# Kernel tuning notes

Measured on AMD Instinct MI355X. Metric: run time of the kernel, lower is better.

The kernel has to match this reference:

```python
import jax, jax.numpy as jnp
import numpy as np

H = 8          # kernel_size == hidden size
NUM_LAYERS = 4
NEG_SLOPE = 0.2


def _gru_scan(x_pre, W_hh, b_hh, reverse):
    """Run a single-direction GRU over time.
    x_pre: (N, T, 3H) precomputed input projections W_ih @ x + b_ih.
    Returns outputs (N, T, H) aligned with input time order.
    PyTorch gate order: [r, z, n].
    """
    N = x_pre.shape[0]

    def step(h, xp):
        gh = h @ W_hh.T + b_hh                      # (N, 3H)
        xr, xz, xn = jnp.split(xp, 3, axis=-1)
        hr, hz, hn = jnp.split(gh, 3, axis=-1)
        r = jax.nn.sigmoid(xr + hr)
        z = jax.nn.sigmoid(xz + hz)
        n = jnp.tanh(xn + r * hn)
        h_new = (1.0 - z) * n + z * h
        return h_new, h_new

    h0 = jnp.zeros((N, H), x_pre.dtype)
    _, ys = jax.lax.scan(step, h0, jnp.swapaxes(x_pre, 0, 1), reverse=reverse)
    return jnp.swapaxes(ys, 0, 1)                   # (N, T, H)


def setup_inputs() -> dict:
    key = jax.random.key(0)
    ks = jax.random.split(key, 16)
    s = 1.0 / np.sqrt(H)  # PyTorch GRU init scale
    u = lambda k, shape: jax.random.uniform(k, shape, jnp.float32, -s, s)
    return {
        "raw": jax.random.normal(ks[0], (32, 400, 4096), jnp.float32),
        "W_ih_l0": u(ks[1], (2, 3 * H, H)),
        "W_hh_l0": u(ks[2], (2, 3 * H, H)),
        "b_ih_l0": u(ks[3], (2, 3 * H)),
        "b_hh_l0": u(ks[4], (2, 3 * H)),
        "W_ih_rest": u(ks[5], (NUM_LAYERS - 1, 2, 3 * H, 2 * H)),
        "W_hh_rest": u(ks[6], (NUM_LAYERS - 1, 2, 3 * H, H)),
        "b_ih_rest": u(ks[7], (NUM_LAYERS - 1, 2, 3 * H)),
        "b_hh_rest": u(ks[8], (NUM_LAYERS - 1, 2, 3 * H)),
        "lin1_w": u(ks[9], (H, 2 * H)),
        "lin1_b": u(ks[10], (H,)),
        "lin2_w": u(ks[11], (H, H)),
        "lin2_b": u(ks[12], (H,)),
    }


def reference(raw, W_ih_l0, W_hh_l0, b_ih_l0, b_hh_l0,
              W_ih_rest, W_hh_rest, b_ih_rest, b_hh_rest,
              lin1_w, lin1_b, lin2_w, lin2_b):
    b, k, L = raw.shape
    T = L // H
    x = raw.reshape(b * k, T, H)                    # (N, T, H)

    for layer in range(NUM_LAYERS):
        if layer == 0:
            Wih, Whh, bih, bhh = W_ih_l0, W_hh_l0, b_ih_l0, b_hh_l0
        else:
            Wih, Whh = W_ih_rest[layer - 1], W_hh_rest[layer - 1]
            bih, bhh = b_ih_rest[layer - 1], b_hh_rest[layer - 1]
        # precompute input projections for the whole sequence (batched GEMM)
        out_f = _gru_scan(x @ Wih[0].T + bih[0], Whh[0], bhh[0], reverse=False)
        out_b = _gru_scan(x @ Wih[1].T + bih[1], Whh[1], bhh[1], reverse=True)
        x = jnp.concatenate([out_f, out_b], axis=-1)  # (N, T, 2H)

    last = x[:, -1, :].reshape(b, k, 2 * H)
    # Dropout is identity in eval mode.
    h = last @ lin1_w.T + lin1_b
    h = jnp.where(h >= 0, h, NEG_SLOPE * h)         # LeakyReLU(0.2)
    return h @ lin2_w.T + lin2_b                    # (b, k, out_size)
```

## Files before the change

kernel.cpp:

```cpp
#include <hip/hip_runtime.h>
#include <type_traits>

#define DEVINL __device__ __forceinline__

typedef __fp16 f16;
typedef __fp16 f16x2 __attribute__((ext_vector_type(2)));
typedef __fp16 f16x8 __attribute__((ext_vector_type(8)));

constexpr int Hh = 8;
constexpr int G3 = 24;
constexpr int TT = 512;

constexpr float SNEG  = -1.44269504088896340736f;
constexpr float SNEG2 = -2.88539008177792681472f;

DEVINL float dot2(f16x2 a, f16x2 b, float c) {
#if __has_builtin(__builtin_amdgcn_fdot2)
    return __builtin_amdgcn_fdot2(a, b, c, false);
#else
    return fmaf((float)a[1], (float)b[1], fmaf((float)a[0], (float)b[0], c));
#endif
}

template <typename InT, bool TWO_IN>
DEVINL void load_x(f16x2* d, const InT* pf, const InT* pb) {
    if constexpr (std::is_same<InT, float>::value) {
        const float4* p4 = (const float4*)pf;
        float4 v0 = p4[0], v1 = p4[1];
        d[0] = __builtin_amdgcn_cvt_pkrtz(v0.x, v0.y);
        d[1] = __builtin_amdgcn_cvt_pkrtz(v0.z, v0.w);
        d[2] = __builtin_amdgcn_cvt_pkrtz(v1.x, v1.y);
        d[3] = __builtin_amdgcn_cvt_pkrtz(v1.z, v1.w);
    } else {
        f16x8 a = *(const f16x8*)pf;
        d[0] = __builtin_shufflevector(a, a, 0, 1);
        d[1] = __builtin_shufflevector(a, a, 2, 3);
        d[2] = __builtin_shufflevector(a, a, 4, 5);
        d[3] = __builtin_shufflevector(a, a, 6, 7);
        if constexpr (TWO_IN) {
            f16x8 b = *(const f16x8*)pb;
            d[4] = __builtin_shufflevector(b, b, 0, 1);
            d[5] = __builtin_shufflevector(b, b, 2, 3);
            d[6] = __builtin_shufflevector(b, b, 4, 5);
            d[7] = __builtin_shufflevector(b, b, 6, 7);
        }
    }
}

template <typename InT, bool TWO_IN, bool LAST>
__global__ __launch_bounds__(128, 4) void gru_scan(
    const InT* __restrict__ xf,
    const InT* __restrict__ xb,
    const float* __restrict__ Wih,
    const float* __restrict__ Whh,
    const float* __restrict__ bih,
    const float* __restrict__ bhh,
    f16* __restrict__ outF,
    f16* __restrict__ outB,
    float* __restrict__ last,
    int n)
{
    constexpr int IN_DIM = TWO_IN ? 16 : 8;
    constexpr int QW = IN_DIM / 2;

    const int tid   = threadIdx.x;
    const int lane8 = tid & 7;
    const int grp   = tid >> 3;
    const int unit  = blockIdx.x * 16 + grp;
    const int dir   = unit >= n ? 1 : 0;
    const int seq   = unit - dir * n;

    const int g0 = lane8, g1 = 8 + lane8, g2 = 16 + lane8;

    __shared__ __align__(16) f16 hsh[128];
    const int hbase = grp * 8;

    const float* Wd = Wih + (size_t)dir * G3 * IN_DIM;
    f16x2 wi0[QW], wi1[QW], wi2[QW];
#pragma unroll
    for (int q = 0; q < QW; ++q) {
        wi0[q] = __builtin_amdgcn_cvt_pkrtz(Wd[g0 * IN_DIM + 2 * q] * SNEG,
                                            Wd[g0 * IN_DIM + 2 * q + 1] * SNEG);
        wi1[q] = __builtin_amdgcn_cvt_pkrtz(Wd[g1 * IN_DIM + 2 * q] * SNEG,
                                            Wd[g1 * IN_DIM + 2 * q + 1] * SNEG);
        wi2[q] = __builtin_amdgcn_cvt_pkrtz(Wd[g2 * IN_DIM + 2 * q] * SNEG2,
                                            Wd[g2 * IN_DIM + 2 * q + 1] * SNEG2);
    }
    const float* Hd = Whh + (size_t)dir * G3 * Hh;
    f16x2 wh0[Hh / 2], wh1[Hh / 2], wh2[Hh / 2];
#pragma unroll
    for (int q = 0; q < Hh / 2; ++q) {
        wh0[q] = __builtin_amdgcn_cvt_pkrtz(Hd[g0 * Hh + 2 * q] * SNEG,
                                            Hd[g0 * Hh + 2 * q + 1] * SNEG);
        wh1[q] = __builtin_amdgcn_cvt_pkrtz(Hd[g1 * Hh + 2 * q] * SNEG,
                                            Hd[g1 * Hh + 2 * q + 1] * SNEG);
        wh2[q] = __builtin_amdgcn_cvt_pkrtz(Hd[g2 * Hh + 2 * q] * SNEG2,
                                            Hd[g2 * Hh + 2 * q + 1] * SNEG2);
    }
    const float br  = (bih[dir * G3 + g0] + bhh[dir * G3 + g0]) * SNEG;
    const float bz  = (bih[dir * G3 + g1] + bhh[dir * G3 + g1]) * SNEG;
    const float bxn = bih[dir * G3 + g2] * SNEG2;
    const float bhn = bhh[dir * G3 + g2] * SNEG2;

    f16x2 h2[Hh / 2];
#pragma unroll
    for (int q = 0; q < Hh / 2; ++q) h2[q] = f16x2{(f16)0.f, (f16)0.f};
    float hown = 0.f;

    const int t0 = dir ? (TT - 1) : 0;
    const int xstep = dir ? -8 : 8;
    const int ostep = dir ? -8 : 8;
    const InT* xpf = xf + (size_t)(seq * TT + t0) * 8;
    const InT* xpb = TWO_IN ? (xb + (size_t)(seq * TT + t0) * 8)
                            : (const InT*)nullptr;
    f16* op = LAST ? nullptr
                   : (dir ? outB : outF) + (size_t)(seq * TT + t0) * 8 + lane8;

    const int steps = (LAST && dir) ? 1 : TT;

    f16x2 xA[QW], xB[QW];
    load_x<InT, TWO_IN>(xA, xpf, xpb);
    xpf += xstep; if constexpr (TWO_IN) xpb += xstep;
    if (steps > 1) {
        load_x<InT, TWO_IN>(xB, xpf, xpb);
        xpf += xstep; if constexpr (TWO_IN) xpb += xstep;
    }

#define GRU_STEP(XV, PF)                                                      \
    {                                                                         \
        float sr = br, sz = bz, xn = bxn;                                     \
        _Pragma("unroll")                                                     \
        for (int q = 0; q < QW; ++q) {                                        \
            sr = dot2(wi0[q], XV[q], sr);                                     \
            sz = dot2(wi1[q], XV[q], sz);                                     \
            xn = dot2(wi2[q], XV[q], xn);                                     \
        }                                                                     \
        if (PF) {                                                             \
            load_x<InT, TWO_IN>(XV, xpf, xpb);                                \
            xpf += xstep; if constexpr (TWO_IN) xpb += xstep;                 \
        }                                                                     \
        float hn = bhn;                                                       \
        _Pragma("unroll")                                                     \
        for (int q = 0; q < Hh / 2; ++q) {                                    \
            sr = dot2(wh0[q], h2[q], sr);                                     \
            sz = dot2(wh1[q], h2[q], sz);                                     \
            hn = dot2(wh2[q], h2[q], hn);                                     \
        }                                                                     \
        float r  = __builtin_amdgcn_rcpf(1.f + __builtin_amdgcn_exp2f(sr));   \
        float z  = __builtin_amdgcn_rcpf(1.f + __builtin_amdgcn_exp2f(sz));   \
        float vS = fminf(fmaf(r, hn, xn), 60.f);               \
        float e2 = __builtin_amdgcn_exp2f(vS);                                \
        float nn = (1.f - e2) * __builtin_amdgcn_rcpf(1.f + e2);              \
        float hnew = fmaf(z, hown - nn, nn);               \
        hown = hnew;                                                          \
        f16 hf = (f16)hnew;                           \
        if (!LAST) { *op = hf; op += ostep; }                                 \
        hsh[hbase + lane8] = hf;                                              \
        __builtin_amdgcn_wave_barrier();                                      \
        f16x8 hv = *(const f16x8*)&hsh[hbase];                                \
        h2[0] = __builtin_shufflevector(hv, hv, 0, 1);                        \
        h2[1] = __builtin_shufflevector(hv, hv, 2, 3);                        \
        h2[2] = __builtin_shufflevector(hv, hv, 4, 5);                        \
        h2[3] = __builtin_shufflevector(hv, hv, 6, 7);                        \
    }

    int s = 0;
    for (; s + 2 < steps; s += 2) {
        GRU_STEP(xA, true);
        GRU_STEP(xB, true);
    }
    GRU_STEP(xA, false);
    if (steps > 1) GRU_STEP(xB, false);
#undef GRU_STEP

    if (LAST) last[(size_t)seq * 16 + dir * 8 + lane8] = hown;
}

__global__ void head_kernel(const float* __restrict__ last,
                            const float* __restrict__ w1, const float* __restrict__ b1,
                            const float* __restrict__ w2, const float* __restrict__ b2,
                            float* __restrict__ out, int n)
{
    int i = blockIdx.x * blockDim.x + threadIdx.x;
    if (i >= n) return;
    const float* v = last + (size_t)i * 16;
    float h1[8];
#pragma unroll
    for (int j = 0; j < 8; ++j) {
        float a = b1[j];
#pragma unroll
        for (int k = 0; k < 16; ++k) a = fmaf(w1[j * 16 + k], v[k], a);
        h1[j] = a >= 0.f ? a : 0.2f * a;
    }
#pragma unroll
    for (int j = 0; j < 8; ++j) {
        float o = b2[j];
#pragma unroll
        for (int k = 0; k < 8; ++k) o = fmaf(w2[j * 8 + k], h1[k], o);
        out[(size_t)i * 8 + j] = o;
    }
}

extern "C" void kernel_launch(void* const* d_in, const int* in_sizes, int n_in,
                              void* d_out, int out_size, void* d_ws, size_t ws_size,
                              hipStream_t stream)
{
    const float* raw  = (const float*)d_in[0];
    const float* Wih0 = (const float*)d_in[1];
    const float* Whh0 = (const float*)d_in[2];
    const float* bih0 = (const float*)d_in[3];
    const float* bhh0 = (const float*)d_in[4];
    const float* WihR = (const float*)d_in[5];
    const float* WhhR = (const float*)d_in[6];
    const float* bihR = (const float*)d_in[7];
    const float* bhhR = (const float*)d_in[8];
    const float* w1   = (const float*)d_in[9];
    const float* b1   = (const float*)d_in[10];
    const float* w2   = (const float*)d_in[11];
    const float* b2   = (const float*)d_in[12];

    const int n = in_sizes[0] / (TT * Hh);
    const size_t hbE = (size_t)n * TT * 8;
    dim3 blk(128);
    dim3 grid((unsigned)((2 * n) / 16));
    dim3 hblk(256);
    dim3 hgrid((unsigned)((n + 255) / 256));

    f16* AF = (f16*)d_ws;
    f16* AB = AF + hbE;
    f16* BF = AB + hbE;
    f16* BB = BF + hbE;
    float* lastb = (float*)(BB + hbE);

    gru_scan<float, false, false><<<grid, blk, 0, stream>>>(
        raw, (const float*)nullptr, Wih0, Whh0, bih0, bhh0,
        AF, AB, (float*)nullptr, n);
    gru_scan<f16, true, false><<<grid, blk, 0, stream>>>(
        AF, AB, WihR + 0 * 2 * G3 * 16, WhhR + 0 * 2 * G3 * 8,
        bihR + 0 * 2 * G3, bhhR + 0 * 2 * G3, BF, BB, (float*)nullptr, n);
    gru_scan<f16, true, false><<<grid, blk, 0, stream>>>(
        BF, BB, WihR + 1 * 2 * G3 * 16, WhhR + 1 * 2 * G3 * 8,
        bihR + 1 * 2 * G3, bhhR + 1 * 2 * G3, AF, AB, (float*)nullptr, n);
    gru_scan<f16, true, true><<<grid, blk, 0, stream>>>(
        AF, AB, WihR + 2 * 2 * G3 * 16, WhhR + 2 * 2 * G3 * 8,
        bihR + 2 * 2 * G3, bhhR + 2 * 2 * G3,
        (f16*)nullptr, (f16*)nullptr, lastb, n);
    head_kernel<<<hgrid, hblk, 0, stream>>>(
        lastb, w1, b1, w2, b2, (float*)d_out, n);
}
```

Baseline: 1.375 ms.

## Process two sequences per thread group to interleave independent GRU recurrences

Each 8-lane group now advances two independent sequences at once. Blocks drop to 64 threads, and each block still covers 16 units. Interleaving the two dependency chains is meant to hide the latency of the serial dot/exp/rcp/LDS chain through ILP. The cost is fewer waves and higher register pressure per thread, with launch bounds changed to (64,2), which may reduce occupancy. Offsets now use 32-bit ints.

After: 1.422 ms. +3.4%, slower.

```diff
diff --git a/kernel.cpp b/kernel.cpp
--- a/kernel.cpp
+++ b/kernel.cpp
@@ -48,7 +48,7 @@
 }
 
 template <typename InT, bool TWO_IN, bool LAST>
-__global__ __launch_bounds__(128, 4) void gru_scan(
+__global__ __launch_bounds__(64, 2) void gru_scan(
     const InT* __restrict__ xf,
     const InT* __restrict__ xb,
     const float* __restrict__ Wih,
@@ -62,18 +62,20 @@
 {
     constexpr int IN_DIM = TWO_IN ? 16 : 8;
     constexpr int QW = IN_DIM / 2;
+    constexpr int XD = TT * 8;
 
     const int tid   = threadIdx.x;
     const int lane8 = tid & 7;
     const int grp   = tid >> 3;
-    const int unit  = blockIdx.x * 16 + grp;
-    const int dir   = unit >= n ? 1 : 0;
-    const int seq   = unit - dir * n;
+    const int unit0 = blockIdx.x * 16 + grp * 2;
+    const int dir   = unit0 >= n ? 1 : 0;
+    const int seq0  = unit0 - dir * n;
 
     const int g0 = lane8, g1 = 8 + lane8, g2 = 16 + lane8;
 
     __shared__ __align__(16) f16 hsh[128];
-    const int hbase = grp * 8;
+    const int hb0 = grp * 16;
+    const int hb1 = grp * 16 + 8;
 
     const float* Wd = Wih + (size_t)dir * G3 * IN_DIM;
     f16x2 wi0[QW], wi1[QW], wi2[QW];
@@ -102,78 +104,104 @@
     const float bxn = bih[dir * G3 + g2] * SNEG2;
     const float bhn = bhh[dir * G3 + g2] * SNEG2;
 
-    f16x2 h2[Hh / 2];
-#pragma unroll
-    for (int q = 0; q < Hh / 2; ++q) h2[q] = f16x2{(f16)0.f, (f16)0.f};
-    float hown = 0.f;
+    f16x2 h20[Hh / 2], h21[Hh / 2];
+#pragma unroll
+    for (int q = 0; q < Hh / 2; ++q) {
+        h20[q] = f16x2{(f16)0.f, (f16)0.f};
+        h21[q] = f16x2{(f16)0.f, (f16)0.f};
+    }
+    float hown0 = 0.f, hown1 = 0.f;
 
     const int t0 = dir ? (TT - 1) : 0;
     const int xstep = dir ? -8 : 8;
     const int ostep = dir ? -8 : 8;
-    const InT* xpf = xf + (size_t)(seq * TT + t0) * 8;
-    const InT* xpb = TWO_IN ? (xb + (size_t)(seq * TT + t0) * 8)
-                            : (const InT*)nullptr;
-    f16* op = LAST ? nullptr
-                   : (dir ? outB : outF) + (size_t)(seq * TT + t0) * 8 + lane8;
+    int xoff = (seq0 * TT + t0) * 8;
+    int ooff = (seq0 * TT + t0) * 8 + lane8;
+    f16* oP = LAST ? nullptr : (dir ? outB : outF);
 
     const int steps = (LAST && dir) ? 1 : TT;
 
-    f16x2 xA[QW], xB[QW];
-    load_x<InT, TWO_IN>(xA, xpf, xpb);
-    xpf += xstep; if constexpr (TWO_IN) xpb += xstep;
+    f16x2 xA0[QW], xA1[QW], xB0[QW], xB1[QW];
+    load_x<InT, TWO_IN>(xA0, xf + xoff, xb + xoff);
+    load_x<InT, TWO_IN>(xA1, xf + xoff + XD, xb + xoff + XD);
+    xoff += xstep;
     if (steps > 1) {
-        load_x<InT, TWO_IN>(xB, xpf, xpb);
-        xpf += xstep; if constexpr (TWO_IN) xpb += xstep;
-    }
-
-#define GRU_STEP(XV, PF)                                                      \
+        load_x<InT, TWO_IN>(xB0, xf + xoff, xb + xoff);
+        load_x<InT, TWO_IN>(xB1, xf + xoff + XD, xb + xoff + XD);
+        xoff += xstep;
+    }
+
+#define GRU_STEP(X0, X1, PF)                                                  \
     {                                                                         \
-        float sr = br, sz = bz, xn = bxn;                                     \
+        float sr0 = br, sz0 = bz, xn0 = bxn;                                  \
+        float sr1 = br, sz1 = bz, xn1 = bxn;                                  \
         _Pragma("unroll")                                                     \
         for (int q = 0; q < QW; ++q) {                                        \
-            sr = dot2(wi0[q], XV[q], sr);                                     \
-            sz = dot2(wi1[q], XV[q], sz);                                     \
-            xn = dot2(wi2[q], XV[q], xn);                                     \
+            sr0 = dot2(wi0[q], X0[q], sr0);                                   \
+            sz0 = dot2(wi1[q], X0[q], sz0);                                   \
+            xn0 = dot2(wi2[q], X0[q], xn0);                                   \
+            sr1 = dot2(wi0[q], X1[q], sr1);                                   \
+            sz1 = dot2(wi1[q], X1[q], sz1);                                   \
+            xn1 = dot2(wi2[q], X1[q], xn1);                                   \
         }                                                                     \
         if (PF) {                                                             \
-            load_x<InT, TWO_IN>(XV, xpf, xpb);                                \
-            xpf += xstep; if constexpr (TWO_IN) xpb += xstep;                 \
+            load_x<InT, TWO_IN>(X0, xf + xoff, xb + xoff);                    \
+            load_x<InT, TWO_IN>(X1, xf + xoff + XD, xb + xoff + XD);          \
+            xoff += xstep;                                                    \
         }                                                                     \
-        float hn = bhn;                                                       \
+        float hn0 = bhn, hn1 = bhn;                                           \
         _Pragma("unroll")                                                     \
         for (int q = 0; q < Hh / 2; ++q) {                                    \
-            sr = dot2(wh0[q], h2[q], sr);                                     \
-            sz = dot2(wh1[q], h2[q], sz);                                     \
-            hn = dot2(wh2[q], h2[q], hn);                                     \
+            sr0 = dot2(wh0[q], h20[q], sr0);                                  \
+            sz0 = dot2(wh1[q], h20[q], sz0);                                  \
+            hn0 = dot2(wh2[q], h20[q], hn0);                                  \
+            sr1 = dot2(wh0[q], h21[q], sr1);                                  \
+            sz1 = dot2(wh1[q], h21[q], sz1);                                  \
+            hn1 = dot2(wh2[q], h21[q], hn1);                                  \
         }                                                                     \
-        float r  = __builtin_amdgcn_rcpf(1.f + __builtin_amdgcn_exp2f(sr));   \
-        float z  = __builtin_amdgcn_rcpf(1.f + __builtin_amdgcn_exp2f(sz));   \
-        float vS = fminf(fmaf(r, hn, xn), 60.f);               \
-        float e2 = __builtin_amdgcn_exp2f(vS);                                \
-        float nn = (1.f - e2) * __builtin_amdgcn_rcpf(1.f + e2);              \
-        float hnew = fmaf(z, hown - nn, nn);               \
-        hown = hnew;                                                          \
-        f16 hf = (f16)hnew;                           \
-        if (!LAST) { *op = hf; op += ostep; }                                 \
-        hsh[hbase + lane8] = hf;                                              \
+        float r0 = __builtin_amdgcn_rcpf(1.f + __builtin_amdgcn_exp2f(sr0));  \
+        float r1 = __builtin_amdgcn_rcpf(1.f + __builtin_amdgcn_exp2f(sr1));  \
+        float z0 = __builtin_amdgcn_rcpf(1.f + __builtin_amdgcn_exp2f(sz0));  \
+        float z1 = __builtin_amdgcn_rcpf(1.f + __builtin_amdgcn_exp2f(sz1));  \
+        float v0 = fminf(fmaf(r0, hn0, xn0), 60.f);            \
+        float v1 = fminf(fmaf(r1, hn1, xn1), 60.f);                           \
+        float e0 = __builtin_amdgcn_exp2f(v0);                                \
+        float e1 = __builtin_amdgcn_exp2f(v1);                                \
+        float nn0 = (1.f - e0) * __builtin_amdgcn_rcpf(1.f + e0);             \
+        float nn1 = (1.f - e1) * __builtin_amdgcn_rcpf(1.f + e1);             \
+        float hA = fmaf(z0, hown0 - nn0, nn0);             \
+        float hB = fmaf(z1, hown1 - nn1, nn1);                                \
+        hown0 = hA; hown1 = hB;                                               \
+        f16 hf0 = (f16)hA, hf1 = (f16)hB;                                     \
+        if (!LAST) { oP[ooff] = hf0; oP[ooff + XD] = hf1; ooff += ostep; }    \
+        hsh[hb0 + lane8] = hf0;                                               \
+        hsh[hb1 + lane8] = hf1;                                               \
         __builtin_amdgcn_wave_barrier();                                      \
-        f16x8 hv = *(const f16x8*)&hsh[hbase];                                \
-        h2[0] = __builtin_shufflevector(hv, hv, 0, 1);                        \
-        h2[1] = __builtin_shufflevector(hv, hv, 2, 3);                        \
-        h2[2] = __builtin_shufflevector(hv, hv, 4, 5);                        \
-        h2[3] = __builtin_shufflevector(hv, hv, 6, 7);                        \
+        f16x8 hv0 = *(const f16x8*)&hsh[hb0];                                 \
+        f16x8 hv1 = *(const f16x8*)&hsh[hb1];                                 \
+        h20[0] = __builtin_shufflevector(hv0, hv0, 0, 1);                     \
+        h20[1] = __builtin_shufflevector(hv0, hv0, 2, 3);                     \
+        h20[2] = __builtin_shufflevector(hv0, hv0, 4, 5);                     \
+        h20[3] = __builtin_shufflevector(hv0, hv0, 6, 7);                     \
+        h21[0] = __builtin_shufflevector(hv1, hv1, 0, 1);                     \
+        h21[1] = __builtin_shufflevector(hv1, hv1, 2, 3);                     \
+        h21[2] = __builtin_shufflevector(hv1, hv1, 4, 5);                     \
+        h21[3] = __builtin_shufflevector(hv1, hv1, 6, 7);                     \
     }
 
     int s = 0;
     for (; s + 2 < steps; s += 2) {
-        GRU_STEP(xA, true);
-        GRU_STEP(xB, true);
-    }
-    GRU_STEP(xA, false);
-    if (steps > 1) GRU_STEP(xB, false);
+        GRU_STEP(xA0, xA1, true);
+        GRU_STEP(xB0, xB1, true);
+    }
+    GRU_STEP(xA0, xA1, false);
+    if (steps > 1) GRU_STEP(xB0, xB1, false);
 #undef GRU_STEP
 
-    if (LAST) last[(size_t)seq * 16 + dir * 8 + lane8] = hown;
+    if (LAST) {
+        last[(size_t)seq0 * 16 + dir * 8 + lane8] = hown0;
+        last[(size_t)(seq0 + 1) * 16 + dir * 8 + lane8] = hown1;
+    }
 }
 
 __global__ void head_kernel(const float* __restrict__ last,
@@ -221,7 +249,7 @@
 
     const int n = in_sizes[0] / (TT * Hh);
     const size_t hbE = (size_t)n * TT * 8;
-    dim3 blk(128);
+    dim3 blk(64);
     dim3 grid((unsigned)((2 * n) / 16));
     dim3 hblk(256);
     dim3 hgrid((unsigned)((n + 255) / 256));
```
